# Kernel tuning notes

Measured on AMD Instinct MI355X. Metric: run time of the kernel, lower is better.

The kernel has to match this reference:

```python
import jax, jax.numpy as jnp
import numpy as np

GRID = 8
NMS_SIZE = 4
TOP_K = 1000
DET_THRESH = 0.015
EPS = 1e-5


def _conv(x, w, b):
    # NCHW, OIHW, SAME padding, stride 1
    y = jax.lax.conv_general_dilated(x, w, (1, 1), 'SAME',
                                     dimension_numbers=('NCHW', 'OIHW', 'NCHW'))
    return y + b[None, :, None, None]


def _bn(x, gamma, beta, mean, var):
    inv = gamma / jnp.sqrt(var + EPS)
    return x * inv[None, :, None, None] + (beta - mean * inv)[None, :, None, None]


def _pixel_shuffle1(x, r):
    # x: [B, r*r, h, w] -> [B, h*r, w*r]  (C_out = 1, squeezed)
    B, C, h, w = x.shape
    x = x.reshape(B, r, r, h, w)
    x = x.transpose(0, 3, 1, 4, 2)  # B, h, r, w, r
    return x.reshape(B, h * r, w * r)


def _box_nms_batched(prob):
    # local-max suppression in a (2*size+1) window + keep top_k scores
    win = 2 * NMS_SIZE + 1
    pooled = jax.lax.reduce_window(prob, -jnp.inf, jax.lax.max,
                                   (1, win, win), (1, 1, 1), 'SAME')
    keep = jnp.where(prob == pooled, prob, 0.0)
    B = keep.shape[0]
    flat = keep.reshape(B, -1)
    kth = jax.lax.top_k(flat, TOP_K)[0][:, -1]  # [B]
    flat = jnp.where(flat >= kth[:, None], flat, 0.0)
    return flat.reshape(prob.shape)


def setup_inputs() -> dict:
    key = jax.random.key(0)
    ks = jax.random.split(key, 5)
    c_in, c_hid = 128, 256
    c_out = GRID * GRID + 1  # 65
    x = jax.random.normal(ks[0], (32, c_in, 60, 80), dtype=jnp.float32)
    wa = jax.random.normal(ks[1], (c_hid, c_in, 3, 3), dtype=jnp.float32) * 0.05
    ba = jnp.zeros((c_hid,), jnp.float32)
    ga = jnp.ones((c_hid,), jnp.float32)
    bta = jnp.zeros((c_hid,), jnp.float32)
    ma = jnp.zeros((c_hid,), jnp.float32)
    va = jnp.ones((c_hid,), jnp.float32)
    wb = jax.random.normal(ks[2], (c_out, c_hid, 1, 1), dtype=jnp.float32) * 0.05
    bb = jnp.zeros((c_out,), jnp.float32)
    gb = jnp.ones((c_out,), jnp.float32)
    btb = jnp.zeros((c_out,), jnp.float32)
    mb = jnp.zeros((c_out,), jnp.float32)
    vb = jnp.ones((c_out,), jnp.float32)
    return {"x": x, "wa": wa, "ba": ba, "ga": ga, "bta": bta, "ma": ma, "va": va,
            "wb": wb, "bb": bb, "gb": gb, "btb": btb, "mb": mb, "vb": vb}


def reference(x, wa, ba, ga, bta, ma, va, wb, bb, gb, btb, mb, vb):
    # convPa: conv3x3 + BN + ReLU
    h = jax.nn.relu(_bn(_conv(x, wa, ba), ga, bta, ma, va))
    # convPb: conv1x1 + BN (no activation)
    logits = _bn(_conv(h, wb, bb), gb, btb, mb, vb)  # [B, 65, h, w]
    # NOTE: original code computes softmax then overwrites it with raw logits
    # (x_prob = self.softmax(x); x_prob = x[:, :-1]) -- we reproduce that bug.
    _ = jax.nn.softmax(logits, axis=1)
    prob = _pixel_shuffle1(logits[:, :-1, :, :], GRID)  # [B, H, W]
    prob_nms = _box_nms_batched(prob)
    pred = (prob_nms >= DET_THRESH).astype(jnp.int32)
    return logits, prob, prob_nms, pred
```

## Files before the change

### kernel.cpp

```cpp
#include <hip/hip_runtime.h>
#include <math.h>

typedef short s16x8 __attribute__((ext_vector_type(8)));
typedef float f32x4 __attribute__((ext_vector_type(4)));
typedef unsigned short u16;

#define B_    32
#define CIN   128
#define CHID  256
#define H_    60
#define W_    80
#define COUT  65
#define HP    480
#define WP    640
#define TOPK  1000
#define CAND_MAX 8192
#define DET_THRESH 0.015f

#define LOGITS_N (B_*COUT*H_*W_)
#define PROB_N   (B_*HP*WP)
#define PROB_OFF (LOGITS_N)
#define NMS_OFF  (PROB_OFF + PROB_N)
#define PRED_OFF (NMS_OFF + PROB_N)

#define WB_FN    442368
#define SA_OFF   WB_FN
#define TA_OFF   (SA_OFF + 256)
#define TB_OFF   (TA_OFF + 256)
#define WB1_FN   30720
#define WB1_OFF  (TB_OFF + 128)
#define H_OFF    (WB1_OFF + WB1_FN)
#define H_N      (B_*H_*W_*CHID)
#define CAND_OFF (H_OFF + H_N)
#define CNT_OFF  (CAND_OFF + B_*CAND_MAX)
#define CNT_N    (32*32)
#define KTH_OFF  (CNT_OFF + CNT_N)
#define WT_N     (CHID*CIN*9)
#define WB1_U16N 61440

#define AROW  58
#define APLN  6264

__device__ __forceinline__ u16 f2bf(float x) {
    unsigned u = __float_as_uint(x);
    return (u16)((u + 0x7fffu + ((u >> 16) & 1u)) >> 16);
}
__device__ __forceinline__ float bf2f(u16 h) {
    return __uint_as_float(((unsigned)h) << 16);
}

#define MFMA16 __builtin_amdgcn_mfma_f32_16x16x32_bf16

__global__ void prep_kernel(const float* __restrict__ wa,
                            const float* __restrict__ ba, const float* __restrict__ ga,
                            const float* __restrict__ bta, const float* __restrict__ ma,
                            const float* __restrict__ va,
                            const float* __restrict__ wb, const float* __restrict__ bb,
                            const float* __restrict__ gb, const float* __restrict__ btb,
                            const float* __restrict__ mb, const float* __restrict__ vb,
                            u16* __restrict__ WBo,
                            float* __restrict__ sa, float* __restrict__ ta,
                            float* __restrict__ tb, u16* __restrict__ WB1o)
{
    int gid = blockIdx.x * 256 + threadIdx.x;
    if (gid < WT_N) {
        int icl = gid & 31;
        int ocl = (gid >> 5) & 63;
        int rest = gid >> 11;
        int tap = rest % 9;
        int cq = rest / 9;
        int icc = cq & 3, ocq = cq >> 2;
        float v = wa[(((ocq * 64 + ocl) * CIN) + icc * 32 + icl) * 9 + tap];
        u16 hh = f2bf(v); float r1 = v - bf2f(hh);
        u16 mm2 = f2bf(r1); float r2 = r1 - bf2f(mm2);
        u16 ll = f2bf(r2);
        size_t base = ((size_t)(((ocq * 4 + icc) * 9 + tap) * 3)) * 2048
                      + ocl * 32 + icl;
        WBo[base] = hh;
        WBo[base + 2048] = mm2;
        WBo[base + 4096] = ll;
    } else if (gid < WT_N + 256) {
        int oc = gid - WT_N;
        float inv = ga[oc] / sqrtf(va[oc] + 1e-5f);
        sa[oc] = inv;
        ta[oc] = (ba[oc] - ma[oc]) * inv + bta[oc];
    } else if (gid < WT_N + 256 + COUT) {
        int oc = gid - (WT_N + 256);
        float inv = gb[oc] / sqrtf(vb[oc] + 1e-5f);
        tb[oc] = (bb[oc] - mb[oc]) * inv + btb[oc];
    } else if (gid < WT_N + 256 + COUT + WB1_U16N) {
        int idx = gid - (WT_N + 256 + COUT);
        int within = idx & 511;
        int j = within & 7;
        int lane = within >> 3;
        int chunk = idx >> 9;
        int plane = chunk % 3;
        int kc = (chunk / 3) & 7;
        int ocf = chunk / 24;
        int oc = ocf * 16 + (lane & 15);
        int k = kc * 32 + (lane >> 4) * 8 + j;
        float v = 0.f;
        if (oc < COUT) {
            float inv = gb[oc] / sqrtf(vb[oc] + 1e-5f);
            v = wb[oc * CHID + k] * inv;
        }
        u16 hh = f2bf(v); float r1 = v - bf2f(hh);
        u16 mm2 = f2bf(r1); float r2 = r1 - bf2f(mm2);
        u16 ll = f2bf(r2);
        WB1o[idx] = (plane == 0) ? hh : (plane == 1) ? mm2 : ll;
    }
}

__global__ __launch_bounds__(256, 2) void conv3_kernel(const float* __restrict__ x,
                                                       const u16* __restrict__ WB,
                                                       const float* __restrict__ sa,
                                                       const float* __restrict__ ta,
                                                       float* __restrict__ h)
{
    __shared__ __align__(16) u16 xsA[3 * APLN];

    int d = blockIdx.x;
    int o = (d & 7) * 300 + (d >> 3);
    int tile = o % 75;
    int b = o / 75;
    int ty = tile / 5, tx = tile % 5;
    int y0 = ty * 4, x0 = tx * 16;

    int t = threadIdx.x;
    int wv = __builtin_amdgcn_readfirstlane(t >> 6);
    int lane = t & 63;
    int cx = lane & 15;
    int kg = lane >> 4;
    int icl0 = kg * 8;

    const float* xb = x + (size_t)b * CIN * H_ * W_;

    int goff[14];
#pragma unroll
    for (int j = 0; j < 14; ++j) {
        int e = t + j * 256;
        int go = -1;
        if (e < 3456) {
            int xx = e % 18;
            int yy = (e / 18) % 6;
            int icl = e / 108;
            int gy = y0 + yy - 1, gx = x0 + xx - 1;
            if (gy >= 0 && gy < H_ && gx >= 0 && gx < W_)
                go = icl * (H_ * W_) + gy * W_ + gx;
        }
        goff[j] = go;
    }

    f32x4 acc[4][4];
#pragma unroll
    for (int pb = 0; pb < 4; ++pb)
#pragma unroll
        for (int f = 0; f < 4; ++f) acc[pb][f] = (f32x4)(0.f);

    float xr[14];
#pragma unroll
    for (int j = 0; j < 14; ++j)
        xr[j] = (goff[j] >= 0) ? xb[goff[j]] : 0.f;

#pragma unroll 1
    for (int icc = 0; icc < 4; ++icc) {
        __syncthreads();
#pragma unroll
        for (int j = 0; j < 14; ++j) {
            int e = t + j * 256;
            if (e < 3456) {
                int xx = e % 18;
                int yy = (e / 18) % 6;
                int icl = e / 108;
                float v = xr[j];
                u16 hh = f2bf(v); float r1 = v - bf2f(hh);
                u16 mm2 = f2bf(r1); float r2 = r1 - bf2f(mm2);
                u16 ll = f2bf(r2);
                int pos = yy * 18 + xx;
                int wu = pos * AROW + ((icl >> 3) << 4) + (icl & 7);
                xsA[wu] = hh;
                xsA[APLN + wu] = mm2;
                xsA[2 * APLN + wu] = ll;
            }
        }
        __syncthreads();

        if (icc < 3) {
            const float* xc = xb + (icc + 1) * 32 * (H_ * W_);
#pragma unroll
            for (int j = 0; j < 14; ++j)
                if (goff[j] >= 0) xr[j] = xc[goff[j]];
        }

#pragma unroll 1
        for (int tap = 0; tap < 9; ++tap) {
            int dy = tap / 3, dx = tap - dy * 3;

            const u16* bb_ = WB + ((size_t)(((wv * 4 + icc) * 9 + tap) * 3)) * 2048;
            s16x8 Bh[4], Bm[4], Bl[4];
#pragma unroll
            for (int f = 0; f < 4; ++f) {
                int bu = (f * 16 + cx) * 32 + icl0;
                Bh[f] = *(const s16x8*)&bb_[bu];
                Bm[f] = *(const s16x8*)&bb_[2048 + bu];
                Bl[f] = *(const s16x8*)&bb_[4096 + bu];
            }

#pragma unroll
            for (int pb = 0; pb < 4; ++pb) {
                int pos = (pb + dy) * 18 + cx + dx;
                int au = pos * AROW + (kg << 4);
                s16x8 Ah = *(const s16x8*)&xsA[au];
                s16x8 Am = *(const s16x8*)&xsA[APLN + au];
                s16x8 Al = *(const s16x8*)&xsA[2 * APLN + au];
#pragma unroll
                for (int f = 0; f < 4; ++f) {
                    acc[pb][f] = MFMA16(Ah, Bh[f], acc[pb][f], 0, 0, 0);
                    acc[pb][f] = MFMA16(Ah, Bm[f], acc[pb][f], 0, 0, 0);
                    acc[pb][f] = MFMA16(Am, Bh[f], acc[pb][f], 0, 0, 0);
                    acc[pb][f] = MFMA16(Ah, Bl[f], acc[pb][f], 0, 0, 0);
                    acc[pb][f] = MFMA16(Am, Bm[f], acc[pb][f], 0, 0, 0);
                    acc[pb][f] = MFMA16(Al, Bh[f], acc[pb][f], 0, 0, 0);
                }
            }
        }
    }

#pragma unroll
    for (int f = 0; f < 4; ++f) {
        int oc = wv * 64 + f * 16 + cx;
        float s_ = sa[oc], t_ = ta[oc];
#pragma unroll
        for (int pb = 0; pb < 4; ++pb) {
            int y = y0 + pb;
#pragma unroll
            for (int r = 0; r < 4; ++r) {
                int xc2 = x0 + kg * 4 + r;
                size_t addr = ((size_t)(b * (H_ * W_) + y * W_ + xc2)) * CHID + oc;
                h[addr] = fmaxf(fmaf(acc[pb][f][r], s_, t_), 0.f);
            }
        }
    }
}

__global__ __launch_bounds__(256) void conv1_kernel(const float* __restrict__ h,
                                                    const u16* __restrict__ WB1,
                                                    const float* __restrict__ tb,
                                                    float* __restrict__ logits,
                                                    float* __restrict__ prob)
{
    __shared__ __align__(16) float hs2[80 * 131];
    int t = threadIdx.x;
    int wv = t >> 6;
    int lane = t & 63;
    int cx = lane & 15;
    int kg = lane >> 4;
    int px0 = blockIdx.x * 128 + wv * 32;

    const float* hp0 = h + (size_t)(px0 + cx) * CHID + kg * 8;
    const float* hp1 = hp0 + 16 * CHID;

    f32x4 acc0[5], acc1[5];
#pragma unroll
    for (int f = 0; f < 5; ++f) { acc0[f] = (f32x4)(0.f); acc1[f] = (f32x4)(0.f); }

#pragma unroll 1
    for (int kc = 0; kc < 8; ++kc) {
        s16x8 Ah0, Am0, Al0, Ah1, Am1, Al1;
        {
            float4 a0 = *(const float4*)(hp0 + kc * 32);
            float4 a1 = *(const float4*)(hp0 + kc * 32 + 4);
            float av[8] = {a0.x, a0.y, a0.z, a0.w, a1.x, a1.y, a1.z, a1.w};
#pragma unroll
            for (int j = 0; j < 8; ++j) {
                u16 hh = f2bf(av[j]); float r1 = av[j] - bf2f(hh);
                u16 mm2 = f2bf(r1); float r2 = r1 - bf2f(mm2);
                Ah0[j] = (short)hh; Am0[j] = (short)mm2; Al0[j] = (short)f2bf(r2);
            }
        }
        {
            float4 a0 = *(const float4*)(hp1 + kc * 32);
            float4 a1 = *(const float4*)(hp1 + kc * 32 + 4);
            float av[8] = {a0.x, a0.y, a0.z, a0.w, a1.x, a1.y, a1.z, a1.w};
#pragma unroll
            for (int j = 0; j < 8; ++j) {
                u16 hh = f2bf(av[j]); float r1 = av[j] - bf2f(hh);
                u16 mm2 = f2bf(r1); float r2 = r1 - bf2f(mm2);
                Ah1[j] = (short)hh; Am1[j] = (short)mm2; Al1[j] = (short)f2bf(r2);
            }
        }
#pragma unroll
        for (int f = 0; f < 5; ++f) {
            const u16* bbase = WB1 + ((size_t)(f * 8 + kc) * 3) * 512 + lane * 8;
            s16x8 Bh = *(const s16x8*)bbase;
            s16x8 Bm = *(const s16x8*)(bbase + 512);
            s16x8 Bl = *(const s16x8*)(bbase + 1024);
            acc0[f] = MFMA16(Ah0, Bh, acc0[f], 0, 0, 0);
            acc0[f] = MFMA16(Ah0, Bm, acc0[f], 0, 0, 0);
            acc0[f] = MFMA16(Am0, Bh, acc0[f], 0, 0, 0);
            acc0[f] = MFMA16(Ah0, Bl, acc0[f], 0, 0, 0);
            acc0[f] = MFMA16(Am0, Bm, acc0[f], 0, 0, 0);
            acc0[f] = MFMA16(Al0, Bh, acc0[f], 0, 0, 0);
            acc1[f] = MFMA16(Ah1, Bh, acc1[f], 0, 0, 0);
            acc1[f] = MFMA16(Ah1, Bm, acc1[f], 0, 0, 0);
            acc1[f] = MFMA16(Am1, Bh, acc1[f], 0, 0, 0);
            acc1[f] = MFMA16(Ah1, Bl, acc1[f], 0, 0, 0);
            acc1[f] = MFMA16(Am1, Bm, acc1[f], 0, 0, 0);
            acc1[f] = MFMA16(Al1, Bh, acc1[f], 0, 0, 0);
        }
    }

#pragma unroll
    for (int f = 0; f < 5; ++f) {
        int oc = f * 16 + cx;
        float tbv = (oc < COUT) ? tb[oc] : 0.f;
#pragma unroll
        for (int r = 0; r < 4; ++r) {
            int pl = wv * 32 + kg * 4 + r;
            hs2[oc * 131 + pl] = acc0[f][r] + tbv;
            hs2[oc * 131 + pl + 16] = acc1[f][r] + tbv;
        }
    }
    __syncthreads();

    int p0 = blockIdx.x * 128;

    for (int e = t; e < 65 * 128; e += 256) {
        int px = e & 127;
        int oc = e >> 7;
        int p = p0 + px;
        int b = p / (H_ * W_);
        int yx = p - b * (H_ * W_);
        logits[((size_t)(b * COUT + oc)) * (H_ * W_) + yx] = hs2[oc * 131 + px];
    }

    for (int e = t; e < 8 * 128; e += 256) {
        int px = e & 127;
        int r1 = e >> 7;
        int p = p0 + px;
        int b = p / (H_ * W_);
        int yx = p - b * (H_ * W_);
        int y = yx / W_, xx = yx - y * W_;
        float4 v0, v1;
        v0.x = hs2[(r1 * 8 + 0) * 131 + px];
        v0.y = hs2[(r1 * 8 + 1) * 131 + px];
        v0.z = hs2[(r1 * 8 + 2) * 131 + px];
        v0.w = hs2[(r1 * 8 + 3) * 131 + px];
        v1.x = hs2[(r1 * 8 + 4) * 131 + px];
        v1.y = hs2[(r1 * 8 + 5) * 131 + px];
        v1.z = hs2[(r1 * 8 + 6) * 131 + px];
        v1.w = hs2[(r1 * 8 + 7) * 131 + px];
        float* dst = prob + (size_t)b * (HP * WP) + (y * 8 + r1) * WP + xx * 8;
        *(float4*)dst = v0;
        *(float4*)(dst + 4) = v1;
    }
}

__global__ __launch_bounds__(256) void nms_kernel(const float* __restrict__ prob,
                                                  float* __restrict__ keep_out,
                                                  float* __restrict__ cand,
                                                  int* __restrict__ cnt)
{
    __shared__ float xs[40][40];
    __shared__ float rmax[40][32];
    __shared__ float clist[1024];
    __shared__ int csh;
    __shared__ int gbase;

    int bid = blockIdx.x;
    int tx = bid % 20;
    int ty = (bid / 20) % 15;
    int b = bid / 300;
    const float* pb = prob + (size_t)b * (HP * WP);
    int t = threadIdx.x;

    if (t == 0) csh = 0;

    for (int idx = t; idx < 1600; idx += 256) {
        int c = idx % 40, r = idx / 40;
        int gy = ty * 32 - 4 + r;
        int gx = tx * 32 - 4 + c;
        float v = -INFINITY;
        if (gy >= 0 && gy < HP && gx >= 0 && gx < WP) v = pb[gy * WP + gx];
        xs[r][c] = v;
    }
    __syncthreads();

    for (int idx = t; idx < 1280; idx += 256) {
        int c = idx & 31, r = idx >> 5;
        float m = xs[r][c];
#pragma unroll
        for (int d = 1; d < 9; ++d) m = fmaxf(m, xs[r][c + d]);
        rmax[r][c] = m;
    }
    __syncthreads();

    for (int idx = t; idx < 1024; idx += 256) {
        int c = idx & 31, ro = idx >> 5;
        float m = rmax[ro][c];
#pragma unroll
        for (int d = 1; d < 9; ++d) m = fmaxf(m, rmax[ro + d][c]);
        float v = xs[ro + 4][c + 4];
        float keep = (v == m) ? v : 0.f;
        keep_out[(size_t)b * (HP * WP) + (ty * 32 + ro) * WP + tx * 32 + c] = keep;
        if (keep > 0.f) {
            int i = atomicAdd(&csh, 1);
            clist[i] = keep;
        }
    }
    __syncthreads();

    int m = csh;
    if (m > 0) {
        if (t == 0) gbase = atomicAdd(&cnt[b * 32], m);
        __syncthreads();
        int gb = gbase;
        for (int i = t; i < m; i += 256) {
            int dst = gb + i;
            if (dst < CAND_MAX) cand[b * CAND_MAX + dst] = clist[i];
        }
    }
}

__global__ __launch_bounds__(256) void select_kernel(const float* __restrict__ cand,
                                                     const int* __restrict__ cnt,
                                                     float* __restrict__ kth)
{
    __shared__ unsigned hist[256];
    __shared__ unsigned sh_prefix, sh_K;

    int b = blockIdx.x;
    int t = threadIdx.x;
    int n = cnt[b * 32];
    if (n > CAND_MAX) n = CAND_MAX;
    if (n < TOPK) {
        if (t == 0) kth[b] = 0.f;
        return;
    }
    if (t == 0) { sh_prefix = 0u; sh_K = TOPK; }
    __syncthreads();
    const float* cb = cand + b * CAND_MAX;

    for (int pass = 3; pass >= 0; --pass) {
        hist[t] = 0u;
        __syncthreads();
        unsigned prefix = sh_prefix;
        unsigned himask = (pass == 3) ? 0u : (0xFFFFFFFFu << ((pass + 1) * 8));
        for (int i = t; i < n; i += 256) {
            unsigned u = __float_as_uint(cb[i]);
            if ((u & himask) == prefix)
                atomicAdd(&hist[(u >> (pass * 8)) & 255], 1u);
        }
        __syncthreads();
        if (t == 0) {
            unsigned K = sh_K, cum = 0;
            int sel = 0;
            for (int v2 = 255; v2 >= 0; --v2) {
                if (cum + hist[v2] >= K) { sel = v2; sh_K = K - cum; break; }
                cum += hist[v2];
            }
            sh_prefix = prefix | ((unsigned)sel << (pass * 8));
        }
        __syncthreads();
    }
    if (t == 0) kth[b] = __uint_as_float(sh_prefix);
}

__global__ __launch_bounds__(256) void thresh_kernel(const float* __restrict__ keep,
                                                     const float* __restrict__ kth,
                                                     float* __restrict__ prob_nms,
                                                     float* __restrict__ pred)
{
    int i4 = blockIdx.x * 256 + threadIdx.x;
    int b = i4 / (HP * WP / 4);
    float tv = kth[b];
    float4 v = ((const float4*)keep)[i4];
    float4 o;
    o.x = (v.x >= tv) ? v.x : 0.f;
    o.y = (v.y >= tv) ? v.y : 0.f;
    o.z = (v.z >= tv) ? v.z : 0.f;
    o.w = (v.w >= tv) ? v.w : 0.f;
    ((float4*)prob_nms)[i4] = o;
    float4 pr;
    pr.x = (o.x >= DET_THRESH) ? 1.f : 0.f;
    pr.y = (o.y >= DET_THRESH) ? 1.f : 0.f;
    pr.z = (o.z >= DET_THRESH) ? 1.f : 0.f;
    pr.w = (o.w >= DET_THRESH) ? 1.f : 0.f;
    ((float4*)pred)[i4] = pr;
}

extern "C" void kernel_launch(void* const* d_in, const int* in_sizes, int n_in,
                              void* d_out, int out_size, void* d_ws, size_t ws_size,
                              hipStream_t stream) {
    const float* x   = (const float*)d_in[0];
    const float* wa  = (const float*)d_in[1];
    const float* ba  = (const float*)d_in[2];
    const float* ga  = (const float*)d_in[3];
    const float* bta = (const float*)d_in[4];
    const float* ma  = (const float*)d_in[5];
    const float* va  = (const float*)d_in[6];
    const float* wb  = (const float*)d_in[7];
    const float* bb  = (const float*)d_in[8];
    const float* gb  = (const float*)d_in[9];
    const float* btb = (const float*)d_in[10];
    const float* mb  = (const float*)d_in[11];
    const float* vb  = (const float*)d_in[12];

    float* out = (float*)d_out;
    float* ws  = (float*)d_ws;

    u16*   WB   = (u16*)ws;
    float* sa   = ws + SA_OFF;
    float* ta   = ws + TA_OFF;
    float* tbv  = ws + TB_OFF;
    u16*   WB1  = (u16*)(ws + WB1_OFF);
    float* h    = ws + H_OFF;
    float* cand = ws + CAND_OFF;
    int*   cnt  = (int*)(ws + CNT_OFF);
    float* kth  = ws + KTH_OFF;

    hipMemsetAsync((void*)cnt, 0, CNT_N * sizeof(int), stream);

    {
        int total = WT_N + 256 + COUT + WB1_U16N;
        prep_kernel<<<(total + 255) / 256, 256, 0, stream>>>(
            wa, ba, ga, bta, ma, va, wb, bb, gb, btb, mb, vb, WB, sa, ta, tbv, WB1);
    }

    conv3_kernel<<<2400, 256, 0, stream>>>(x, WB, sa, ta, h);

    conv1_kernel<<<(B_ * H_ * W_) / 128, 256, 0, stream>>>(
        h, WB1, tbv, out, out + PROB_OFF);

    nms_kernel<<<32 * 15 * 20, 256, 0, stream>>>(
        out + PROB_OFF, out + NMS_OFF, cand, cnt);

    select_kernel<<<B_, 256, 0, stream>>>(cand, cnt, kth);

    thresh_kernel<<<(PROB_N / 4) / 256, 256, 0, stream>>>(
        out + NMS_OFF, kth, out + NMS_OFF, out + PRED_OFF);
}
```

Baseline: 571.0 us.

## Double-buffer conv3x3 input tile in LDS and overlap staging with MFMA taps

```diff
diff --git a/kernel.cpp b/kernel.cpp
--- a/kernel.cpp
+++ b/kernel.cpp
@@ -117,7 +117,7 @@
                                                        const float* __restrict__ ta,
                                                        float* __restrict__ h)
 {
-    __shared__ __align__(16) u16 xsA[3 * APLN];
+    __shared__ __align__(16) u16 xsA[2][3 * APLN];
 
     int d = blockIdx.x;
     int o = (d & 7) * 300 + (d >> 3);
@@ -161,29 +161,30 @@
 #pragma unroll
     for (int j = 0; j < 14; ++j)
         xr[j] = (goff[j] >= 0) ? xb[goff[j]] : 0.f;
+#pragma unroll
+    for (int j = 0; j < 14; ++j) {
+        int e = t + j * 256;
+        if (e < 3456) {
+            int xx = e % 18;
+            int yy = (e / 18) % 6;
+            int icl = e / 108;
+            float v = xr[j];
+            u16 hh = f2bf(v); float r1 = v - bf2f(hh);
+            u16 mm2 = f2bf(r1); float r2 = r1 - bf2f(mm2);
+            u16 ll = f2bf(r2);
+            int pos = yy * 18 + xx;
+            int wu = pos * AROW + ((icl >> 3) << 4) + (icl & 7);
+            xsA[0][wu] = hh;
+            xsA[0][APLN + wu] = mm2;
+            xsA[0][2 * APLN + wu] = ll;
+        }
+    }
+    __syncthreads();
 
 #pragma unroll 1
     for (int icc = 0; icc < 4; ++icc) {
-        __syncthreads();
-#pragma unroll
-        for (int j = 0; j < 14; ++j) {
-            int e = t + j * 256;
-            if (e < 3456) {
-                int xx = e % 18;
-                int yy = (e / 18) % 6;
-                int icl = e / 108;
-                float v = xr[j];
-                u16 hh = f2bf(v); float r1 = v - bf2f(hh);
-                u16 mm2 = f2bf(r1); float r2 = r1 - bf2f(mm2);
-                u16 ll = f2bf(r2);
-                int pos = yy * 18 + xx;
-                int wu = pos * AROW + ((icl >> 3) << 4) + (icl & 7);
-                xsA[wu] = hh;
-                xsA[APLN + wu] = mm2;
-                xsA[2 * APLN + wu] = ll;
-            }
-        }
-        __syncthreads();
+        int cur = icc & 1;
+        const u16* xa = xsA[cur];
 
         if (icc < 3) {
             const float* xc = xb + (icc + 1) * 32 * (H_ * W_);
@@ -193,9 +194,8 @@
         }
 
 #pragma unroll 1
-        for (int tap = 0; tap < 9; ++tap) {
+        for (int tap = 0; tap < 4; ++tap) {
             int dy = tap / 3, dx = tap - dy * 3;
-
             const u16* bb_ = WB + ((size_t)(((wv * 4 + icc) * 9 + tap) * 3)) * 2048;
             s16x8 Bh[4], Bm[4], Bl[4];
 #pragma unroll
@@ -205,14 +205,13 @@
                 Bm[f] = *(const s16x8*)&bb_[2048 + bu];
                 Bl[f] = *(const s16x8*)&bb_[4096 + bu];
             }
-
 #pragma unroll
             for (int pb = 0; pb < 4; ++pb) {
                 int pos = (pb + dy) * 18 + cx + dx;
                 int au = pos * AROW + (kg << 4);
-                s16x8 Ah = *(const s16x8*)&xsA[au];
-                s16x8 Am = *(const s16x8*)&xsA[APLN + au];
-                s16x8 Al = *(const s16x8*)&xsA[2 * APLN + au];
+                s16x8 Ah = *(const s16x8*)&xa[au];
+                s16x8 Am = *(const s16x8*)&xa[APLN + au];
+                s16x8 Al = *(const s16x8*)&xa[2 * APLN + au];
 #pragma unroll
                 for (int f = 0; f < 4; ++f) {
                     acc[pb][f] = MFMA16(Ah, Bh[f], acc[pb][f], 0, 0, 0);
@@ -224,6 +223,61 @@
                 }
             }
         }
+
+        if (icc < 3) {
+            u16* xw = xsA[cur ^ 1];
+#pragma unroll
+            for (int j = 0; j < 14; ++j) {
+                int e = t + j * 256;
+                if (e < 3456) {
+                    int xx = e % 18;
+                    int yy = (e / 18) % 6;
+                    int icl = e / 108;
+                    float v = xr[j];
+                    u16 hh = f2bf(v); float r1 = v - bf2f(hh);
+                    u16 mm2 = f2bf(r1); float r2 = r1 - bf2f(mm2);
+                    u16 ll = f2bf(r2);
+                    int pos = yy * 18 + xx;
+                    int wu = pos * AROW + ((icl >> 3) << 4) + (icl & 7);
+                    xw[wu] = hh;
+                    xw[APLN + wu] = mm2;
+                    xw[2 * APLN + wu] = ll;
+                }
+            }
+        }
+
+#pragma unroll 1
+        for (int tap = 4; tap < 9; ++tap) {
+            int dy = tap / 3, dx = tap - dy * 3;
+            const u16* bb_ = WB + ((size_t)(((wv * 4 + icc) * 9 + tap) * 3)) * 2048;
+            s16x8 Bh[4], Bm[4], Bl[4];
+#pragma unroll
+            for (int f = 0; f < 4; ++f) {
+                int bu = (f * 16 + cx) * 32 + icl0;
+                Bh[f] = *(const s16x8*)&bb_[bu];
+                Bm[f] = *(const s16x8*)&bb_[2048 + bu];
+                Bl[f] = *(const s16x8*)&bb_[4096 + bu];
+            }
+#pragma unroll
+            for (int pb = 0; pb < 4; ++pb) {
+                int pos = (pb + dy) * 18 + cx + dx;
+                int au = pos * AROW + (kg << 4);
+                s16x8 Ah = *(const s16x8*)&xa[au];
+                s16x8 Am = *(const s16x8*)&xa[APLN + au];
+                s16x8 Al = *(const s16x8*)&xa[2 * APLN + au];
+#pragma unroll
+                for (int f = 0; f < 4; ++f) {
+                    acc[pb][f] = MFMA16(Ah, Bh[f], acc[pb][f], 0, 0, 0);
+                    acc[pb][f] = MFMA16(Ah, Bm[f], acc[pb][f], 0, 0, 0);
+                    acc[pb][f] = MFMA16(Am, Bh[f], acc[pb][f], 0, 0, 0);
+                    acc[pb][f] = MFMA16(Ah, Bl[f], acc[pb][f], 0, 0, 0);
+                    acc[pb][f] = MFMA16(Am, Bm[f], acc[pb][f], 0, 0, 0);
+                    acc[pb][f] = MFMA16(Al, Bh[f], acc[pb][f], 0, 0, 0);
+                }
+            }
+        }
+
+        __syncthreads();
     }
 
 #pragma unroll
```

Result: slower. 694.6 us (+21.6%).
